# Kernel tuning notes

Hardware: AMD Instinct MI355X
Metric: run time of the kernel (lower is better)

The kernel has to match this reference:

```python
import jax, jax.numpy as jnp
import numpy as np

B, T, D = 16, 4096, 256
CODEBOOK_SIZE = 1024
COMMITMENT = 1.0


def setup_inputs() -> dict:
    key = jax.random.key(0)
    kx, kc = jax.random.split(key)
    x = jax.random.normal(kx, (B, T, D), dtype=jnp.float32)
    codebook = jax.random.normal(kc, (CODEBOOK_SIZE, D), dtype=jnp.float32)
    return {"x": x, "codebook": codebook}


def reference(x, codebook):
    # x: [B, T, D] continuous latents; codebook: [K, D]
    flat = x.reshape(-1, x.shape[-1])  # [N, D]
    # does not affect argmin but is kept for faithfulness to torch.cdist-style math)
    x_sq = jnp.sum(flat * flat, axis=1, keepdims=True)            # [N, 1]
    c_sq = jnp.sum(codebook * codebook, axis=1)                   # [K]
    dist = x_sq - 2.0 * (flat @ codebook.T) + c_sq[None, :]       # [N, K]
    indices = jnp.argmin(dist, axis=1)                            # [N] int
    quantized = codebook[indices].reshape(x.shape)                # gather, [B, T, D]
    # commitment loss: encoder pulled toward (stopped) codes
    commit_loss = COMMITMENT * jnp.mean(
        (x - jax.lax.stop_gradient(quantized)) ** 2
    )
    # straight-through estimator
    out = x + jax.lax.stop_gradient(quantized - x)
    return out, indices.reshape(x.shape[:-1]), commit_loss
```

## Files before the change

kernel.cpp:

```cpp
#include <hip/hip_runtime.h>

#define N_TOK 65536
#define DIM   256
#define KCODE 1024

#define NTHREADS 256
#define TM 128
#define TN 128
#define BK 32
#define NCHUNK 8
#define NSTAGE 24
#define OTM 128

#define REFINE_EPS 0.125f
#define TIE_THETA 1.0e-4

#define WS_CSQ_OFF   16
#define WS_IDX_OFF   2048
#define WS_PAIRS_OFF (WS_IDX_OFF + N_TOK)
#define WS_CBPK_OFF  (WS_PAIRS_OFF + N_TOK * NCHUNK * 4)

typedef float f32x4  __attribute__((ext_vector_type(4)));
typedef short bf16x8 __attribute__((ext_vector_type(8)));
typedef short s16x8  __attribute__((ext_vector_type(8)));

__global__ void rowsq_np_kernel(const float* __restrict__ m,
                                float* __restrict__ out,
                                float* __restrict__ loss_ws, int rows) {
#pragma clang fp contract(off)
    if (blockIdx.x == 0 && threadIdx.x == 0) loss_ws[0] = 0.0f;
    int row = blockIdx.x * 16 + (threadIdx.x >> 4);
    int l   = threadIdx.x & 15;
    if (row >= rows) return;
    int h = l >> 3;
    int j = l & 7;
    const float* p = m + (size_t)row * DIM + h * 128 + j;
    float v = p[0];
    float r = v * v;
#pragma unroll
    for (int i = 1; i < 16; ++i) {
        float w  = p[i * 8];
        float w2 = w * w;
        r = r + w2;
    }
    float t = r + __shfl_xor(r, 1);
    t = t + __shfl_xor(t, 2);
    t = t + __shfl_xor(t, 4);
    t = t + __shfl_xor(t, 8);
    if (l == 0) out[row] = t;
}

__device__ __forceinline__ void ins2(float d, int idx,
                                     float& d1, int& i1, float& d2, int& i2) {
    if (d < d1 || (d == d1 && idx < i1)) {
        d2 = d1; i2 = i1; d1 = d; i1 = idx;
    } else if ((d < d2 || (d == d2 && idx < i2)) && idx != i1) {
        d2 = d; i2 = idx;
    }
}

__device__ __forceinline__ void f2bf_split(float v, short& hi, short& lo) {
    unsigned u = __float_as_uint(v);
    unsigned r = (u + 0x7fffu + ((u >> 16) & 1u)) >> 16;
    hi = (short)r;
    float hf = __uint_as_float(r << 16);
    float lf = v - hf;
    unsigned u2 = __float_as_uint(lf);
    unsigned r2 = (u2 + 0x7fffu + ((u2 >> 16) & 1u)) >> 16;
    lo = (short)r2;
}

__global__ void pack_tiles_kernel(const float* __restrict__ src,
                                  unsigned short* __restrict__ dst,
                                  int total) {
    int tid = blockIdx.x * blockDim.x + threadIdx.x;
    if (tid >= total) return;
    int s   = tid & 3;
    int r   = (tid >> 2) & 127;
    int kc  = (tid >> 9) & 7;
    int g   = tid >> 12;
    int oct = s ^ ((r >> 1) & 3);

    const float4* xr = reinterpret_cast<const float4*>(
        src + ((size_t)(g * 128 + r)) * DIM + kc * 32 + oct * 8);
    float4 v0 = xr[0];
    float4 v1 = xr[1];

    float f[8] = {v0.x, v0.y, v0.z, v0.w, v1.x, v1.y, v1.z, v1.w};
    s16x8 hv, lv;
#pragma unroll
    for (int i = 0; i < 8; ++i) {
        short h, l;
        f2bf_split(f[i], h, l);
        hv[i] = h; lv[i] = l;
    }
    size_t base_hi = (((size_t)(g * 16 + kc) * 128 + r) << 5) + s * 8;
    size_t base_lo = (((size_t)(g * 16 + 8 + kc) * 128 + r) << 5) + s * 8;
    *reinterpret_cast<s16x8*>(dst + base_hi) = hv;
    *reinterpret_cast<s16x8*>(dst + base_lo) = lv;
}

__device__ __forceinline__ void gload_lds16(const unsigned short* g, unsigned short* lds) {
    __builtin_amdgcn_global_load_lds(
        (const __attribute__((address_space(1))) unsigned int*)g,
        (__attribute__((address_space(3))) unsigned int*)lds, 16, 0, 0);
}

__launch_bounds__(NTHREADS, 3)
__global__ void vq_main_kernel(const unsigned short* __restrict__ xpk,
                               const unsigned short* __restrict__ cbpk,
                               const float* __restrict__ csq,
                               float4* __restrict__ pairs) {
    __shared__ __align__(16) unsigned short shbuf[3][2 * TM * BK];
    __shared__ float4 pairs_sh[TM][2];

    const int tid  = threadIdx.x;
    const int w    = tid >> 6;
    const int wy   = w >> 1;
    const int wx   = w & 1;
    const int lane = tid & 63;
    const int lm   = lane & 15;
    const int q    = lane >> 4;

    const int bx     = blockIdx.x;
    const int jj     = bx >> 3;
    const int grp    = (bx & 7) + ((jj >> 3) << 3);
    const int cchunk = jj & 7;
    const int tok0   = grp * TM;
    const int code0  = cchunk * TN;

    float cs_reg[4];
#pragma unroll
    for (int ni = 0; ni < 4; ++ni)
        cs_reg[ni] = csq[code0 + wx * 64 + ni * 16 + lm];

    f32x4 acc[4][4];
#pragma unroll
    for (int mi = 0; mi < 4; ++mi)
#pragma unroll
        for (int ni = 0; ni < 4; ++ni)
            acc[mi][ni] = (f32x4){0.f, 0.f, 0.f, 0.f};

    int offA[4], offB[4];
#pragma unroll
    for (int mi = 0; mi < 4; ++mi) {
        int r = wy * 64 + mi * 16 + lm;
        offA[mi] = r * BK + ((q ^ ((r >> 1) & 3)) * 8);
    }
#pragma unroll
    for (int ni = 0; ni < 4; ++ni) {
        int r = wx * 64 + ni * 16 + lm;
        offB[ni] = TM * BK + r * BK + ((q ^ ((r >> 1) & 3)) * 8);
    }

    const int lsrc = w * 1024 + lane * 8;
    auto stage = [&](int p, int s) {
        const int seg = s >> 3;
        const int kc  = s & 7;
        const int pa  = (seg == 2) ? 8 : 0;
        const int pb  = (seg == 1) ? 8 : 0;
        const unsigned short* ga = xpk  + (((size_t)(grp    * 16 + pa + kc)) << 12) + lsrc;
        const unsigned short* gb = cbpk + (((size_t)(cchunk * 16 + pb + kc)) << 12) + lsrc;
        unsigned short* At = &shbuf[p][w * 1024];
        unsigned short* Bt = &shbuf[p][TM * BK + w * 1024];
        gload_lds16(ga,       At);
        gload_lds16(ga + 512, At + 512);
        gload_lds16(gb,       Bt);
        gload_lds16(gb + 512, Bt + 512);
    };

    stage(0, 0);
    stage(1, 1);

    int pc = 0;
#pragma unroll 1
    for (int s = 0; s < NSTAGE - 1; ++s) {
        asm volatile("s_waitcnt vmcnt(4)" ::: "memory");
        __builtin_amdgcn_s_barrier();
        __builtin_amdgcn_sched_barrier(0);

        if (s + 2 < NSTAGE) {
            int pn = pc + 2; if (pn >= 3) pn -= 3;
            stage(pn, s + 2);
        }

        const unsigned short* buf = &shbuf[pc][0];
        bf16x8 af[4], bf[4];
#pragma unroll
        for (int mi = 0; mi < 4; ++mi)
            af[mi] = *reinterpret_cast<const bf16x8*>(buf + offA[mi]);
#pragma unroll
        for (int ni = 0; ni < 4; ++ni)
            bf[ni] = *reinterpret_cast<const bf16x8*>(buf + offB[ni]);

        __builtin_amdgcn_s_setprio(1);
#pragma unroll
        for (int mi = 0; mi < 4; ++mi)
#pragma unroll
            for (int ni = 0; ni < 4; ++ni)
                acc[mi][ni] = __builtin_amdgcn_mfma_f32_16x16x32_bf16(
                    af[mi], bf[ni], acc[mi][ni], 0, 0, 0);
        __builtin_amdgcn_s_setprio(0);

        pc = (pc == 2) ? 0 : pc + 1;
    }

    asm volatile("s_waitcnt vmcnt(0)" ::: "memory");
    __builtin_amdgcn_s_barrier();
    __builtin_amdgcn_sched_barrier(0);
    {
        const unsigned short* buf = &shbuf[pc][0];
        bf16x8 af[4], bf[4];
#pragma unroll
        for (int mi = 0; mi < 4; ++mi)
            af[mi] = *reinterpret_cast<const bf16x8*>(buf + offA[mi]);
#pragma unroll
        for (int ni = 0; ni < 4; ++ni)
            bf[ni] = *reinterpret_cast<const bf16x8*>(buf + offB[ni]);
        __builtin_amdgcn_s_setprio(1);
#pragma unroll
        for (int mi = 0; mi < 4; ++mi)
#pragma unroll
            for (int ni = 0; ni < 4; ++ni)
                acc[mi][ni] = __builtin_amdgcn_mfma_f32_16x16x32_bf16(
                    af[mi], bf[ni], acc[mi][ni], 0, 0, 0);
        __builtin_amdgcn_s_setprio(0);
    }

#pragma unroll
    for (int mi = 0; mi < 4; ++mi) {
#pragma unroll
        for (int r = 0; r < 4; ++r) {
            int row_local = wy * 64 + mi * 16 + q * 4 + r;
            float l1 = 3.4e38f, l2 = 3.4e38f;
            int   j1 = 0x7fffffff, j2 = 0x7fffffff;
#pragma unroll
            for (int ni = 0; ni < 4; ++ni) {
                float d = cs_reg[ni] - 2.0f * acc[mi][ni][r];
                ins2(d, code0 + wx * 64 + ni * 16 + lm, l1, j1, l2, j2);
            }
#pragma unroll
            for (int m = 1; m < 16; m <<= 1) {
                float o1 = __shfl_xor(l1, m);
                int   p1 = __shfl_xor(j1, m);
                float o2 = __shfl_xor(l2, m);
                int   p2 = __shfl_xor(j2, m);
                ins2(o1, p1, l1, j1, l2, j2);
                ins2(o2, p2, l1, j1, l2, j2);
            }
            if (lm == 0) {
                float4 pr;
                pr.x = l1; pr.y = l2;
                pr.z = __int_as_float(j1); pr.w = __int_as_float(j2);
                pairs_sh[row_local][wx] = pr;
            }
        }
    }
    __syncthreads();
    if (tid < TM) {
        float4 pa = pairs_sh[tid][0];
        float4 pb = pairs_sh[tid][1];
        float d1 = pa.x, d2 = pa.y;
        int   i1 = __float_as_int(pa.z), i2 = __float_as_int(pa.w);
        ins2(pb.x, __float_as_int(pb.z), d1, i1, d2, i2);
        ins2(pb.y, __float_as_int(pb.w), d1, i1, d2, i2);
        float4 pr;
        pr.x = d1; pr.y = d2;
        pr.z = __int_as_float(i1); pr.w = __int_as_float(i2);
        pairs[(size_t)cchunk * N_TOK + tok0 + tid] = pr;
    }
}

__launch_bounds__(256)
__global__ void merge_output_kernel(const float* __restrict__ x,
                                    const float* __restrict__ cb,
                                    const float4* __restrict__ pairs,
                                    float* __restrict__ out_q,
                                    float* __restrict__ out_idx,
                                    float* __restrict__ loss_ws) {
    __shared__ int   sh_idx[OTM];
    __shared__ float wsum[4];
    const int tid  = threadIdx.x;
    const int tok0 = blockIdx.x * OTM;

    if (tid < OTM) {
        const int t = tok0 + tid;
        float4 p0 = pairs[t];
        float d1 = p0.x, d2 = p0.y;
        int   i1 = __float_as_int(p0.z), i2 = __float_as_int(p0.w);
#pragma unroll
        for (int c = 1; c < NCHUNK; ++c) {
            float4 p = pairs[(size_t)c * N_TOK + t];
            ins2(p.x, __float_as_int(p.z), d1, i1, d2, i2);
            ins2(p.y, __float_as_int(p.w), d1, i1, d2, i2);
        }

        int pick = i1;
        if (d2 - d1 < REFINE_EPS) {
            const float* xr = x + (size_t)t * DIM;
            const float* c1 = cb + (size_t)i1 * DIM;
            const float* c2 = cb + (size_t)i2 * DIM;
            double sA = 0.0, dA = 0.0, sB = 0.0, dB = 0.0;
            for (int k = 0; k < DIM; ++k) {
                double xv = (double)xr[k];
                double a  = (double)c1[k];
                double b  = (double)c2[k];
                sA += a * a; dA += xv * a;
                sB += b * b; dB += xv * b;
            }
            double DA  = sA - 2.0 * dA;
            double DB  = sB - 2.0 * dB;
            double gap = DB - DA;
            if (gap > TIE_THETA)       pick = i1;
            else if (gap < -TIE_THETA) pick = i2;
            else                       pick = (i1 < i2) ? i1 : i2;
        }
        sh_idx[tid] = pick;
        out_idx[t]  = (float)pick;
    }
    __syncthreads();

    float lsum = 0.0f;
    for (int t = 0; t < OTM; ++t) {
        int code = sh_idx[t];
        float qv = cb[(size_t)code * DIM + tid];
        float xv = x[(size_t)(tok0 + t) * DIM + tid];
        out_q[(size_t)(tok0 + t) * DIM + tid] = xv + (qv - xv);
        float df = xv - qv;
        lsum = fmaf(df, df, lsum);
    }

#pragma unroll
    for (int off = 1; off < 64; off <<= 1) lsum += __shfl_xor(lsum, off);
    if ((tid & 63) == 0) wsum[tid >> 6] = lsum;
    __syncthreads();
    if (tid == 0) atomicAdd(loss_ws, (wsum[0] + wsum[1]) + (wsum[2] + wsum[3]));
}

__global__ void finalize_kernel(const float* ws, float* out_loss) {
    if (threadIdx.x == 0) out_loss[0] = ws[0] * (1.0f / 16777216.0f);
}

extern "C" void kernel_launch(void* const* d_in, const int* in_sizes, int n_in,
                              void* d_out, int out_size, void* d_ws, size_t ws_size,
                              hipStream_t stream) {
    const float* x  = (const float*)d_in[0];
    const float* cb = (const float*)d_in[1];

    float* out      = (float*)d_out;
    float* out_q    = out;
    float* out_idx  = out + (size_t)N_TOK * DIM;
    float* out_loss = out_idx + N_TOK;

    float*  ws    = (float*)d_ws;
    float*  csq   = ws + WS_CSQ_OFF;
    float4* pairs = (float4*)(ws + WS_PAIRS_OFF);
    unsigned short* cbpk = (unsigned short*)(ws + WS_CBPK_OFF);
    unsigned short* xpk  = (unsigned short*)out_q;

    rowsq_np_kernel<<<KCODE / 16, 256, 0, stream>>>(cb, csq, ws, KCODE);
    pack_tiles_kernel<<<(N_TOK * 32) / 256, 256, 0, stream>>>(x, xpk, N_TOK * 32);
    pack_tiles_kernel<<<(KCODE * 32) / 256, 256, 0, stream>>>(cb, cbpk, KCODE * 32);
    vq_main_kernel<<<(N_TOK / TM) * NCHUNK, NTHREADS, 0, stream>>>(xpk, cbpk, csq, pairs);
    merge_output_kernel<<<N_TOK / OTM, 256, 0, stream>>>(x, cb, pairs, out_q, out_idx, ws);
    finalize_kernel<<<1, 64, 0, stream>>>(ws, out_loss);
}
```

Before: 816.4 us.

## Load hi/lo bf16 splits together per k-chunk and double-buffer the stages

Restructures the split-bf16 GEMM. It no longer streams 24 separate hi/lo segment stages through a triple buffer. Each k-chunk now loads the A-hi, A-lo, B-hi and B-lo tiles at once into a larger double buffer and issues the three cross-product MFMAs per chunk. This cuts the loop to 8 iterations and reuses each loaded fragment across two products, but it doubles per-block LDS, lowers occupancy to 2 blocks per CU, and replaces the finer vmcnt-based waits with full __syncthreads.

```diff
diff --git a/kernel.cpp b/kernel.cpp
--- a/kernel.cpp
+++ b/kernel.cpp
@@ -9,7 +9,7 @@
 #define TN 128
 #define BK 32
 #define NCHUNK 8
-#define NSTAGE 24
+#define NSTAGE 8
 #define OTM 128
 
 #define REFINE_EPS 0.125f
@@ -106,12 +106,12 @@
         (__attribute__((address_space(3))) unsigned int*)lds, 16, 0, 0);
 }
 
-__launch_bounds__(NTHREADS, 3)
+__launch_bounds__(NTHREADS, 2)
 __global__ void vq_main_kernel(const unsigned short* __restrict__ xpk,
                                const unsigned short* __restrict__ cbpk,
                                const float* __restrict__ csq,
                                float4* __restrict__ pairs) {
-    __shared__ __align__(16) unsigned short shbuf[3][2 * TM * BK];
+    __shared__ __align__(16) unsigned short shbuf[2][4 * 4096];
     __shared__ float4 pairs_sh[TM][2];
 
     const int tid  = threadIdx.x;
@@ -150,48 +150,46 @@
 #pragma unroll
     for (int ni = 0; ni < 4; ++ni) {
         int r = wx * 64 + ni * 16 + lm;
-        offB[ni] = TM * BK + r * BK + ((q ^ ((r >> 1) & 3)) * 8);
+        offB[ni] = r * BK + ((q ^ ((r >> 1) & 3)) * 8);
     }
 
     const int lsrc = w * 1024 + lane * 8;
-    auto stage = [&](int p, int s) {
-        const int seg = s >> 3;
-        const int kc  = s & 7;
-        const int pa  = (seg == 2) ? 8 : 0;
-        const int pb  = (seg == 1) ? 8 : 0;
-        const unsigned short* ga = xpk  + (((size_t)(grp    * 16 + pa + kc)) << 12) + lsrc;
-        const unsigned short* gb = cbpk + (((size_t)(cchunk * 16 + pb + kc)) << 12) + lsrc;
-        unsigned short* At = &shbuf[p][w * 1024];
-        unsigned short* Bt = &shbuf[p][TM * BK + w * 1024];
-        gload_lds16(ga,       At);
-        gload_lds16(ga + 512, At + 512);
-        gload_lds16(gb,       Bt);
-        gload_lds16(gb + 512, Bt + 512);
+    auto stage = [&](int p, int kc) {
+        const unsigned short* gah = xpk  + (((size_t)(grp    * 16 +     kc)) << 12) + lsrc;
+        const unsigned short* gal = xpk  + (((size_t)(grp    * 16 + 8 + kc)) << 12) + lsrc;
+        const unsigned short* gbh = cbpk + (((size_t)(cchunk * 16 +     kc)) << 12) + lsrc;
+        const unsigned short* gbl = cbpk + (((size_t)(cchunk * 16 + 8 + kc)) << 12) + lsrc;
+        unsigned short* base = &shbuf[p][w * 1024];
+        gload_lds16(gah,       base);
+        gload_lds16(gah + 512, base + 512);
+        gload_lds16(gal,       base + 4096);
+        gload_lds16(gal + 512, base + 4096 + 512);
+        gload_lds16(gbh,       base + 8192);
+        gload_lds16(gbh + 512, base + 8192 + 512);
+        gload_lds16(gbl,       base + 12288);
+        gload_lds16(gbl + 512, base + 12288 + 512);
     };
 
     stage(0, 0);
-    stage(1, 1);
-
-    int pc = 0;
+    __syncthreads();
+
+    int p = 0;
 #pragma unroll 1
-    for (int s = 0; s < NSTAGE - 1; ++s) {
-        asm volatile("s_waitcnt vmcnt(4)" ::: "memory");
-        __builtin_amdgcn_s_barrier();
-        __builtin_amdgcn_sched_barrier(0);
-
-        if (s + 2 < NSTAGE) {
-            int pn = pc + 2; if (pn >= 3) pn -= 3;
-            stage(pn, s + 2);
-        }
-
-        const unsigned short* buf = &shbuf[pc][0];
-        bf16x8 af[4], bf[4];
-#pragma unroll
-        for (int mi = 0; mi < 4; ++mi)
-            af[mi] = *reinterpret_cast<const bf16x8*>(buf + offA[mi]);
-#pragma unroll
-        for (int ni = 0; ni < 4; ++ni)
-            bf[ni] = *reinterpret_cast<const bf16x8*>(buf + offB[ni]);
+    for (int kc = 0; kc < NSTAGE; ++kc) {
+        if (kc < NSTAGE - 1) stage(p ^ 1, kc + 1);
+
+        const unsigned short* buf = &shbuf[p][0];
+        bf16x8 ah[4], al[4], bh[4], bl[4];
+#pragma unroll
+        for (int mi = 0; mi < 4; ++mi) {
+            ah[mi] = *reinterpret_cast<const bf16x8*>(buf + offA[mi]);
+            al[mi] = *reinterpret_cast<const bf16x8*>(buf + 4096 + offA[mi]);
+        }
+#pragma unroll
+        for (int ni = 0; ni < 4; ++ni) {
+            bh[ni] = *reinterpret_cast<const bf16x8*>(buf + 8192 + offB[ni]);
+            bl[ni] = *reinterpret_cast<const bf16x8*>(buf + 12288 + offB[ni]);
+        }
 
         __builtin_amdgcn_s_setprio(1);
 #pragma unroll
@@ -199,32 +197,23 @@
 #pragma unroll
             for (int ni = 0; ni < 4; ++ni)
                 acc[mi][ni] = __builtin_amdgcn_mfma_f32_16x16x32_bf16(
-                    af[mi], bf[ni], acc[mi][ni], 0, 0, 0);
-        __builtin_amdgcn_s_setprio(0);
-
-        pc = (pc == 2) ? 0 : pc + 1;
-    }
-
-    asm volatile("s_waitcnt vmcnt(0)" ::: "memory");
-    __builtin_amdgcn_s_barrier();
-    __builtin_amdgcn_sched_barrier(0);
-    {
-        const unsigned short* buf = &shbuf[pc][0];
-        bf16x8 af[4], bf[4];
-#pragma unroll
-        for (int mi = 0; mi < 4; ++mi)
-            af[mi] = *reinterpret_cast<const bf16x8*>(buf + offA[mi]);
-#pragma unroll
-        for (int ni = 0; ni < 4; ++ni)
-            bf[ni] = *reinterpret_cast<const bf16x8*>(buf + offB[ni]);
-        __builtin_amdgcn_s_setprio(1);
+                    ah[mi], bh[ni], acc[mi][ni], 0, 0, 0);
 #pragma unroll
         for (int mi = 0; mi < 4; ++mi)
 #pragma unroll
             for (int ni = 0; ni < 4; ++ni)
                 acc[mi][ni] = __builtin_amdgcn_mfma_f32_16x16x32_bf16(
-                    af[mi], bf[ni], acc[mi][ni], 0, 0, 0);
+                    ah[mi], bl[ni], acc[mi][ni], 0, 0, 0);
+#pragma unroll
+        for (int mi = 0; mi < 4; ++mi)
+#pragma unroll
+            for (int ni = 0; ni < 4; ++ni)
+                acc[mi][ni] = __builtin_amdgcn_mfma_f32_16x16x32_bf16(
+                    al[mi], bh[ni], acc[mi][ni], 0, 0, 0);
         __builtin_amdgcn_s_setprio(0);
+
+        __syncthreads();
+        p ^= 1;
     }
 
 #pragma unroll
```

Measured after the change: 889.1 us. +8.9%, slower.
